# Kernel tuning notes

Measured on AMD Instinct MI355X. Metric: run time of the kernel, lower is better.

The kernel has to match this reference:

```python
import jax, jax.numpy as jnp
import numpy as np

N_EMBD = 1024
HEAD_SIZE = 64
B, T = 4, 4096


def setup_inputs() -> dict:
    key = jax.random.key(0)
    kx, kk, kq, kv = jax.random.split(key, 4)
    s = 1.0 / np.sqrt(N_EMBD)
    return {
        "x": jax.random.normal(kx, (B, T, N_EMBD), dtype=jnp.float32),
        "Wk": jax.random.normal(kk, (N_EMBD, HEAD_SIZE), dtype=jnp.float32) * s,
        "Wq": jax.random.normal(kq, (N_EMBD, HEAD_SIZE), dtype=jnp.float32) * s,
        "Wv": jax.random.normal(kv, (N_EMBD, HEAD_SIZE), dtype=jnp.float32) * s,
    }


def reference(x, Wk, Wq, Wv):
    Bb, Tt, C = x.shape
    k = x @ Wk  # [B,T,H]
    q = x @ Wq
    v = x @ Wv
    # scores scaled by C**-0.5 where C = n_embd (as in the original module)
    w = jnp.einsum('bth,bsh->bts', q, k) * (C ** -0.5)  # [B,T,T]
    causal = jnp.tril(jnp.ones((Tt, Tt), dtype=bool))
    w = jnp.where(causal, w, -jnp.inf)
    w = jax.nn.softmax(w, axis=-1)
    # dropout prob is 0.0 (eval) -> identity
    out = jnp.einsum('bts,bsh->bth', w, v)  # [B,T,H]
    return out
```

## Files before the change

kernel.cpp:

```cpp
#include <hip/hip_runtime.h>


#define BSZ 4
#define TSZ 4096
#define CSZ 1024
#define MSZ (BSZ * TSZ)
#define NS 8
#define QT 128
#define NQT (TSZ / QT)

typedef _Float16 half8 __attribute__((ext_vector_type(8)));
typedef _Float16 half4 __attribute__((ext_vector_type(4)));
typedef float f32x4 __attribute__((ext_vector_type(4)));

#define MFMA(a, b, c) __builtin_amdgcn_mfma_f32_16x16x32_f16((a), (b), (c), 0, 0, 0)
#define QSCALE 0.04508422002778011f

__device__ __forceinline__ int kimg(int r, int h) {
    return r * 64 + ((((h >> 3) ^ (r & 7))) << 3) + (h & 7);
}
__device__ __forceinline__ int vimg(int kk, int h) {
    int p = (kk & 15) * 4 + (kk >> 4);
    return h * 64 + ((((p >> 3) ^ (h & 7))) << 3) + (p & 7);
}

__device__ __forceinline__ void glds16(const _Float16* g, _Float16* l) {
    __builtin_amdgcn_global_load_lds(
        (const __attribute__((address_space(1))) void*)g,
        (__attribute__((address_space(3))) void*)l, 16, 0, 0);
}

__global__ __launch_bounds__(192) void wconv(const float* __restrict__ Wk,
                                             const float* __restrict__ Wq,
                                             const float* __restrict__ Wv,
                                             _Float16* __restrict__ Wt) {
    int kk = blockIdx.x;
    int n = threadIdx.x;
    const float* W = (n < 64) ? Wk : ((n < 128) ? Wq : Wv);
    float v = W[kk * 64 + (n & 63)];
    if (n >= 64 && n < 128) v *= QSCALE;
    Wt[(size_t)n * 1024 + kk] = (_Float16)v;
}

__global__ __launch_bounds__(256) void qkv_proj(const float* __restrict__ x,
                                                const _Float16* __restrict__ Wt,
                                                _Float16* __restrict__ qbf,
                                                _Float16* __restrict__ kbs,
                                                _Float16* __restrict__ vts) {
    __shared__ _Float16 xt[2][32 * 128];

    int tid = threadIdx.x;
    int wave = tid >> 6, lane = tid & 63;
    int quad = lane >> 4, l16 = lane & 15;
    int row0 = blockIdx.x * 32;

    f32x4 acc[6];
#pragma unroll
    for (int i = 0; i < 6; i++) acc[i] = (f32x4){0.f, 0.f, 0.f, 0.f};

    int sr = tid >> 3;
    int sc = tid & 7;
    const float* xrow = x + (size_t)(row0 + sr) * CSZ + sc * 16;

    f32x4 p[4];
#pragma unroll
    for (int i = 0; i < 4; i++) p[i] = *(const f32x4*)(xrow + i * 4);

    int cur = 0;
    for (int kc = 0; kc < CSZ; kc += 128, cur ^= 1) {
        {
            _Float16 tmp[16] __attribute__((aligned(16)));
#pragma unroll
            for (int i = 0; i < 16; i++) tmp[i] = (_Float16)p[i >> 2][i & 3];
            *(half8*)&xt[cur][sr * 128 + ((sc * 2) ^ (sr & 7)) * 8] =
                *(half8*)tmp;
            *(half8*)&xt[cur][sr * 128 + ((sc * 2 + 1) ^ (sr & 7)) * 8] =
                *(half8*)(tmp + 8);
        }
        __syncthreads();
        if (kc + 128 < CSZ) {
#pragma unroll
            for (int i = 0; i < 4; i++)
                p[i] = *(const f32x4*)(xrow + kc + 128 + i * 4);
        }
#pragma unroll
        for (int ss = 0; ss < 4; ss++) {
            half8 a0 = *(half8*)&xt[cur][l16 * 128 +
                                         ((ss * 4 + quad) ^ (l16 & 7)) * 8];
            half8 a1 = *(half8*)&xt[cur][(16 + l16) * 128 +
                                         ((ss * 4 + quad) ^ (l16 & 7)) * 8];
#pragma unroll
            for (int j = 0; j < 3; j++) {
                int ct = wave * 3 + j;
                half8 bb = *(const half8*)&Wt[(size_t)(ct * 16 + l16) * CSZ +
                                              kc + ss * 32 + quad * 8];
                acc[j * 2 + 0] = MFMA(a0, bb, acc[j * 2 + 0]);
                acc[j * 2 + 1] = MFMA(a1, bb, acc[j * 2 + 1]);
            }
        }
    }

#pragma unroll
    for (int j = 0; j < 3; j++) {
        int ct = wave * 3 + j;
        int kind = ct >> 2;
        int col = (ct & 3) * 16 + l16;
#pragma unroll
        for (int m = 0; m < 2; m++) {
#pragma unroll
            for (int r = 0; r < 4; r++) {
                int row = row0 + m * 16 + quad * 4 + r;
                _Float16 val = (_Float16)acc[j * 2 + m][r];
                if (kind == 0) {
                    kbs[((size_t)(row >> 6)) * 4096 + kimg(row & 63, col)] = val;
                } else if (kind == 1) {
                    qbf[(size_t)row * 64 + col] = val;
                } else {
                    vts[((size_t)(row >> 6)) * 4096 + vimg(row & 63, col)] = val;
                }
            }
        }
    }
}

__global__ __launch_bounds__(256) void attn_partial(
    const _Float16* __restrict__ qbf, const _Float16* __restrict__ kbs,
    const _Float16* __restrict__ vts, _Float16* __restrict__ opart,
    float* __restrict__ ml) {
    __shared__ _Float16 kt[2][4096];
    __shared__ _Float16 vt[2][4096];
    __shared__ _Float16 pt[QT * 64];

    int tid = threadIdx.x;
    int wave = tid >> 6, lane = tid & 63;
    int quad = lane >> 4, l16 = lane & 15;
    int s = blockIdx.x & (NS - 1);
    int qt = (blockIdx.x >> 3) & (NQT - 1);
    int b = blockIdx.x >> 8;
    int nt = 2 * (qt + 1);
    int lo = s * nt / NS, hi = (s + 1) * nt / NS;
    int part = (b * NQT + qt) * NS + s;

    if (lo >= hi) {
        if (tid < QT) ml[part * QT + tid] = 0.f;
        return;
    }

    const _Float16* qb = qbf + (size_t)b * TSZ * 64;
    const _Float16* kbs_b = kbs + (size_t)b * 64 * 4096;
    const _Float16* vts_b = vts + (size_t)b * 64 * 4096;

    int qrow = qt * QT + wave * 32;
    half8 aq[2][2];
#pragma unroll
    for (int st = 0; st < 2; st++)
#pragma unroll
        for (int ss = 0; ss < 2; ss++)
            aq[st][ss] = *(const half8*)&qb[(qrow + st * 16 + l16) * 64 +
                                            ss * 32 + quad * 8];

    f32x4 o[2][4];
    float l_acc[2][4];
#pragma unroll
    for (int st = 0; st < 2; st++)
#pragma unroll
        for (int ct = 0; ct < 4; ct++) {
            o[st][ct] = (f32x4){0.f, 0.f, 0.f, 0.f};
            l_acc[st][ct] = 0.f;
        }

    int soff = wave * 512 + lane * 8;

    {
        const _Float16* ks = kbs_b + (size_t)lo * 4096 + soff;
        const _Float16* vs = vts_b + (size_t)lo * 4096 + soff;
        glds16(ks, &kt[0][soff]);
        glds16(ks + 2048, &kt[0][2048 + soff]);
        glds16(vs, &vt[0][soff]);
        glds16(vs + 2048, &vt[0][2048 + soff]);
    }

    int cur = 0;
    for (int kti = lo; kti < hi; kti++, cur ^= 1) {
        __syncthreads();
        if (kti + 1 < hi) {
            const _Float16* ks = kbs_b + (size_t)(kti + 1) * 4096 + soff;
            const _Float16* vs = vts_b + (size_t)(kti + 1) * 4096 + soff;
            glds16(ks, &kt[cur ^ 1][soff]);
            glds16(ks + 2048, &kt[cur ^ 1][2048 + soff]);
            glds16(vs, &vt[cur ^ 1][soff]);
            glds16(vs + 2048, &vt[cur ^ 1][2048 + soff]);
        }

        f32x4 sacc[2][4];
#pragma unroll
        for (int st = 0; st < 2; st++)
#pragma unroll
            for (int ct = 0; ct < 4; ct++)
                sacc[st][ct] = (f32x4){0.f, 0.f, 0.f, 0.f};
#pragma unroll
        for (int ss = 0; ss < 2; ss++) {
#pragma unroll
            for (int ct = 0; ct < 4; ct++) {
                half8 bb = *(half8*)&kt[cur][(ct * 16 + l16) * 64 +
                                             ((ss * 4 + quad) ^ (l16 & 7)) * 8];
                sacc[0][ct] = MFMA(aq[0][ss], bb, sacc[0][ct]);
                sacc[1][ct] = MFMA(aq[1][ss], bb, sacc[1][ct]);
            }
        }

        bool diag = (kti >= 2 * qt);
#pragma unroll
        for (int st = 0; st < 2; st++) {
#pragma unroll
            for (int r = 0; r < 4; r++) {
                int lrow = wave * 32 + st * 16 + quad * 4 + r;
                float pv[4];
#pragma unroll
                for (int ct = 0; ct < 4; ct++) {
                    float e = exp2f(sacc[st][ct][r]);
                    if (diag) {
                        int key = kti * 64 + ct * 16 + l16;
                        if (key > qt * QT + lrow) e = 0.f;
                    }
                    pv[ct] = e;
                }
                l_acc[st][r] += pv[0] + pv[1] + pv[2] + pv[3];
                half4 hp;
#pragma unroll
                for (int ct = 0; ct < 4; ct++) hp[ct] = (_Float16)pv[ct];
                int chunk = (l16 >> 1) ^ (lrow & 7);
                *(half4*)&pt[lrow * 64 + chunk * 8 + (l16 & 1) * 4] = hp;
            }
        }

#pragma unroll
        for (int ss = 0; ss < 2; ss++) {
            half8 ap0 = *(half8*)&pt[(wave * 32 + l16) * 64 +
                                     ((ss * 4 + quad) ^ (l16 & 7)) * 8];
            half8 ap1 = *(half8*)&pt[(wave * 32 + 16 + l16) * 64 +
                                     ((ss * 4 + quad) ^ (l16 & 7)) * 8];
#pragma unroll
            for (int ct = 0; ct < 4; ct++) {
                half8 bv = *(half8*)&vt[cur][(ct * 16 + l16) * 64 +
                                             ((ss * 4 + quad) ^ (l16 & 7)) * 8];
                o[0][ct] = MFMA(ap0, bv, o[0][ct]);
                o[1][ct] = MFMA(ap1, bv, o[1][ct]);
            }
        }
    }

#pragma unroll
    for (int off = 1; off < 16; off <<= 1) {
#pragma unroll
        for (int st = 0; st < 2; st++)
#pragma unroll
            for (int r = 0; r < 4; r++)
                l_acc[st][r] += __shfl_xor(l_acc[st][r], off);
    }

    _Float16* op = opart + (size_t)part * (QT * 64);
#pragma unroll
    for (int st = 0; st < 2; st++) {
#pragma unroll
        for (int r = 0; r < 4; r++) {
            int lrow = wave * 32 + st * 16 + quad * 4 + r;
            float li = l_acc[st][r];
            float inv = li > 0.f ? 1.f / li : 0.f;
#pragma unroll
            for (int ct = 0; ct < 4; ct++)
                op[lrow * 64 + ct * 16 + l16] = (_Float16)(o[st][ct][r] * inv);
            if (l16 == 0) ml[part * QT + lrow] = li;
        }
    }
}

__global__ __launch_bounds__(256) void combine(
    const _Float16* __restrict__ opart, const float* __restrict__ ml,
    float* __restrict__ out) {
    int tid = threadIdx.x;
    int row = blockIdx.x * 32 + (tid >> 3);
    int seg = (tid & 7) * 8;
    int b = row >> 12;
    int qt = (row >> 7) & (NQT - 1);
    int prow = row & (QT - 1);
    int pbase = (b * NQT + qt) * NS;

    float acc[8];
#pragma unroll
    for (int i = 0; i < 8; i++) acc[i] = 0.f;
    float lsum = 0.f;
#pragma unroll
    for (int s = 0; s < NS; s++) {
        float l = ml[(pbase + s) * QT + prow];
        lsum += l;
        half8 h = *(const half8*)&opart[(size_t)(pbase + s) * (QT * 64) +
                                        prow * 64 + seg];
#pragma unroll
        for (int i = 0; i < 8; i++) acc[i] += l * (float)h[i];
    }
    float inv = 1.f / lsum;
    float* ob = out + (size_t)row * 64 + seg;
#pragma unroll
    for (int i = 0; i < 8; i++) ob[i] = acc[i] * inv;
}

extern "C" void kernel_launch(void* const* d_in, const int* in_sizes, int n_in,
                              void* d_out, int out_size, void* d_ws,
                              size_t ws_size, hipStream_t stream) {
    (void)in_sizes; (void)n_in; (void)out_size; (void)ws_size;
    const float* x = (const float*)d_in[0];
    const float* Wk = (const float*)d_in[1];
    const float* Wq = (const float*)d_in[2];
    const float* Wv = (const float*)d_in[3];

    _Float16* Wt = (_Float16*)d_ws;
    _Float16* qbf = Wt + 192 * 1024;
    _Float16* kbs = qbf + (size_t)MSZ * 64;
    _Float16* vts = kbs + (size_t)MSZ * 64;
    _Float16* opart = vts + (size_t)MSZ * 64;
    float* ml = (float*)(opart + (size_t)BSZ * NQT * NS * QT * 64);

    wconv<<<1024, 192, 0, stream>>>(Wk, Wq, Wv, Wt);
    qkv_proj<<<MSZ / 32, 256, 0, stream>>>(x, Wt, qbf, kbs, vts);
    attn_partial<<<BSZ * NQT * NS, 256, 0, stream>>>(qbf, kbs, vts, opart, ml);
    combine<<<MSZ / 32, 256, 0, stream>>>(opart, ml, (float*)d_out);
}
```

Baseline: 162.3 us.

## Stage projection weights in LDS with swizzled layout and double buffering

The QKV projection kernel now stages its fp16 weight tile in shared memory through async global-to-LDS loads, double-buffered across 64-wide K chunks. Previously each wave read weights straight from global memory in the inner loop. The weight conversion kernel pre-swizzles the weight layout so that the LDS reads avoid bank conflicts. The K chunk shrinks from 128 to 64 and launch bounds request 2 blocks per CU, which raises LDS use per block and the number of barriers.

```diff
diff --git a/kernel.cpp b/kernel.cpp
--- a/kernel.cpp
+++ b/kernel.cpp
@@ -17,11 +17,11 @@
 #define QSCALE 0.04508422002778011f
 
 __device__ __forceinline__ int kimg(int r, int h) {
-    return r * 64 + ((((h >> 3) ^ (r & 7))) << 3) + (h & 7);
+    return r * 64 + (((h >> 3) ^ (r & 7)) << 3) + (h & 7);
 }
 __device__ __forceinline__ int vimg(int kk, int h) {
     int p = (kk & 15) * 4 + (kk >> 4);
-    return h * 64 + ((((p >> 3) ^ (h & 7))) << 3) + (p & 7);
+    return h * 64 + (((p >> 3) ^ (h & 7)) << 3) + (p & 7);
 }
 
 __device__ __forceinline__ void glds16(const _Float16* g, _Float16* l) {
@@ -34,20 +34,21 @@
                                              const float* __restrict__ Wq,
                                              const float* __restrict__ Wv,
                                              _Float16* __restrict__ Wt) {
-    int kk = blockIdx.x;
+    int k = blockIdx.x;
     int n = threadIdx.x;
+    int g = k >> 6, c = (k >> 3) & 7, j = k & 7;
     const float* W = (n < 64) ? Wk : ((n < 128) ? Wq : Wv);
-    float v = W[kk * 64 + (n & 63)];
+    float v = W[k * 64 + (n & 63)];
     if (n >= 64 && n < 128) v *= QSCALE;
-    Wt[(size_t)n * 1024 + kk] = (_Float16)v;
-}
-
-__global__ __launch_bounds__(256) void qkv_proj(const float* __restrict__ x,
-                                                const _Float16* __restrict__ Wt,
-                                                _Float16* __restrict__ qbf,
-                                                _Float16* __restrict__ kbs,
-                                                _Float16* __restrict__ vts) {
-    __shared__ _Float16 xt[2][32 * 128];
+    Wt[(size_t)n * 1024 + g * 64 + ((c ^ (n & 7)) << 3) + j] = (_Float16)v;
+}
+
+__global__ __launch_bounds__(256, 2) void qkv_proj(
+    const float* __restrict__ x, const _Float16* __restrict__ Wt,
+    _Float16* __restrict__ qbf, _Float16* __restrict__ kbs,
+    _Float16* __restrict__ vts) {
+    __shared__ _Float16 wt[2][192 * 64];
+    __shared__ _Float16 xt[2][32 * 64];
 
     int tid = threadIdx.x;
     int wave = tid >> 6, lane = tid & 63;
@@ -58,42 +59,54 @@
 #pragma unroll
     for (int i = 0; i < 6; i++) acc[i] = (f32x4){0.f, 0.f, 0.f, 0.f};
 
-    int sr = tid >> 3;
-    int sc = tid & 7;
-    const float* xrow = x + (size_t)(row0 + sr) * CSZ + sc * 16;
-
-    f32x4 p[4];
-#pragma unroll
-    for (int i = 0; i < 4; i++) p[i] = *(const f32x4*)(xrow + i * 4);
+    int sr = tid >> 3, sc = tid & 7;
+    const float* xrow = x + (size_t)(row0 + sr) * CSZ + sc * 8;
+    f32x4 p0 = *(const f32x4*)xrow;
+    f32x4 p1 = *(const f32x4*)(xrow + 4);
+
+#pragma unroll
+    for (int i = 0; i < 6; i++) {
+        int g = i * 256 + tid;
+        glds16(Wt + ((size_t)(g >> 3)) * 1024 + 0 + (g & 7) * 8,
+               &wt[0][(size_t)tid * 8 + i * 2048]);
+    }
 
     int cur = 0;
-    for (int kc = 0; kc < CSZ; kc += 128, cur ^= 1) {
+    for (int kc = 0; kc < CSZ; kc += 64, cur ^= 1) {
         {
-            _Float16 tmp[16] __attribute__((aligned(16)));
-#pragma unroll
-            for (int i = 0; i < 16; i++) tmp[i] = (_Float16)p[i >> 2][i & 3];
-            *(half8*)&xt[cur][sr * 128 + ((sc * 2) ^ (sr & 7)) * 8] =
-                *(half8*)tmp;
-            *(half8*)&xt[cur][sr * 128 + ((sc * 2 + 1) ^ (sr & 7)) * 8] =
-                *(half8*)(tmp + 8);
+            _Float16 tmp[8] __attribute__((aligned(16)));
+#pragma unroll
+            for (int i = 0; i < 4; i++) {
+                tmp[i] = (_Float16)p0[i];
+                tmp[4 + i] = (_Float16)p1[i];
+            }
+            *(half8*)&xt[cur][sr * 64 + ((sc ^ (sr & 7)) << 3)] = *(half8*)tmp;
         }
         __syncthreads();
-        if (kc + 128 < CSZ) {
-#pragma unroll
-            for (int i = 0; i < 4; i++)
-                p[i] = *(const f32x4*)(xrow + kc + 128 + i * 4);
-        }
-#pragma unroll
-        for (int ss = 0; ss < 4; ss++) {
-            half8 a0 = *(half8*)&xt[cur][l16 * 128 +
-                                         ((ss * 4 + quad) ^ (l16 & 7)) * 8];
-            half8 a1 = *(half8*)&xt[cur][(16 + l16) * 128 +
-                                         ((ss * 4 + quad) ^ (l16 & 7)) * 8];
+
+        if (kc + 64 < CSZ) {
+#pragma unroll
+            for (int i = 0; i < 6; i++) {
+                int g = i * 256 + tid;
+                glds16(Wt + ((size_t)(g >> 3)) * 1024 + (kc + 64) + (g & 7) * 8,
+                       &wt[cur ^ 1][(size_t)tid * 8 + i * 2048]);
+            }
+            p0 = *(const f32x4*)(xrow + kc + 64);
+            p1 = *(const f32x4*)(xrow + kc + 68);
+        }
+
+#pragma unroll
+        for (int ss = 0; ss < 2; ss++) {
+            half8 a0 = *(half8*)&xt[cur][l16 * 64 +
+                                         (((ss * 4 + quad) ^ (l16 & 7)) << 3)];
+            half8 a1 = *(half8*)&xt[cur][(16 + l16) * 64 +
+                                         (((ss * 4 + quad) ^ (l16 & 7)) << 3)];
 #pragma unroll
             for (int j = 0; j < 3; j++) {
                 int ct = wave * 3 + j;
-                half8 bb = *(const half8*)&Wt[(size_t)(ct * 16 + l16) * CSZ +
-                                              kc + ss * 32 + quad * 8];
+                half8 bb = *(half8*)&wt[cur][(ct * 16 + l16) * 64 +
+                                             (((ss * 4 + quad) ^ (l16 & 7))
+                                              << 3)];
                 acc[j * 2 + 0] = MFMA(a0, bb, acc[j * 2 + 0]);
                 acc[j * 2 + 1] = MFMA(a1, bb, acc[j * 2 + 1]);
             }
@@ -156,7 +169,7 @@
     for (int st = 0; st < 2; st++)
 #pragma unroll
         for (int ss = 0; ss < 2; ss++)
-            aq[st][ss] = *(const half8*)&qb[(qrow + st * 16 + l16) * 64 +
+            aq[st][ss] = *(const half8*)&qb[(size_t)(qrow + st * 16 + l16) * 64 +
                                             ss * 32 + quad * 8];
 
     f32x4 o[2][4];
@@ -203,7 +216,8 @@
 #pragma unroll
             for (int ct = 0; ct < 4; ct++) {
                 half8 bb = *(half8*)&kt[cur][(ct * 16 + l16) * 64 +
-                                             ((ss * 4 + quad) ^ (l16 & 7)) * 8];
+                                             (((ss * 4 + quad) ^ (l16 & 7))
+                                              << 3)];
                 sacc[0][ct] = MFMA(aq[0][ss], bb, sacc[0][ct]);
                 sacc[1][ct] = MFMA(aq[1][ss], bb, sacc[1][ct]);
             }
@@ -237,13 +251,14 @@
 #pragma unroll
         for (int ss = 0; ss < 2; ss++) {
             half8 ap0 = *(half8*)&pt[(wave * 32 + l16) * 64 +
-                                     ((ss * 4 + quad) ^ (l16 & 7)) * 8];
+                                     (((ss * 4 + quad) ^ (l16 & 7)) << 3)];
             half8 ap1 = *(half8*)&pt[(wave * 32 + 16 + l16) * 64 +
-                                     ((ss * 4 + quad) ^ (l16 & 7)) * 8];
+                                     (((ss * 4 + quad) ^ (l16 & 7)) << 3)];
 #pragma unroll
             for (int ct = 0; ct < 4; ct++) {
                 half8 bv = *(half8*)&vt[cur][(ct * 16 + l16) * 64 +
-                                             ((ss * 4 + quad) ^ (l16 & 7)) * 8];
+                                             (((ss * 4 + quad) ^ (l16 & 7))
+                                              << 3)];
                 o[0][ct] = MFMA(ap0, bv, o[0][ct]);
                 o[1][ct] = MFMA(ap1, bv, o[1][ct]);
             }
```

After: 154.7 us. 1.05x faster.
